# Optimization experiments

Measured on AMD Instinct MI355X. Metric: run time of the kernel, lower is better.

The kernel has to match this reference:

```python
import jax, jax.numpy as jnp
import numpy as np

B, T, N_EMBD, HEAD = 8, 2048, 1024, 64
NEG_INF = -1e30  # stand-in for float('-inf'), safe under fp16/bf16 after where


def setup_inputs() -> dict:
    key = jax.random.key(0)
    k0, k1, k2, k3 = jax.random.split(key, 4)
    idx = jax.random.normal(k0, (B, T, N_EMBD), dtype=jnp.float32)
    # nn.Linear weights have shape (out_features, in_features)
    Wk = jax.random.normal(k1, (HEAD, N_EMBD), dtype=jnp.float32) * 0.02
    Wq = jax.random.normal(k2, (HEAD, N_EMBD), dtype=jnp.float32) * 0.02
    Wv = jax.random.normal(k3, (HEAD, N_EMBD), dtype=jnp.float32) * 0.02
    return {"idx": idx, "Wk": Wk, "Wq": Wq, "Wv": Wv}


def reference(idx, Wk, Wq, Wv):
    # idx: [B,T,C]; W*: [H,C] (torch Linear layout, y = x @ W.T)
    Tn = idx.shape[1]
    k = jnp.einsum('btc,hc->bth', idx, Wk)
    q = jnp.einsum('btc,hc->bth', idx, Wq)
    v = jnp.einsum('btc,hc->bth', idx, Wv)
    # NOTE: original has NO 1/sqrt(head_size) scaling
    wei = jnp.einsum('bth,bsh->bts', q, k)  # [B,T,T]
    causal = jnp.tril(jnp.ones((Tn, Tn), dtype=bool))  # keep where tril != 0
    wei = jnp.where(causal[None, :, :], wei, NEG_INF)
    # NOTE: original softmaxes over dim=1 (query axis), not the last axis
    wei = jax.nn.softmax(wei, axis=1)
    out = jnp.einsum('bts,bsh->bth', wei, v)  # [B,T,H]
    return out
```

## Files before the change

kernel.cpp:

```cpp
#include <hip/hip_runtime.h>


typedef __attribute__((ext_vector_type(8))) short bf16x8;
typedef __attribute__((ext_vector_type(4))) float f32x4;
typedef unsigned short u16;

#define MFMA(a, b, c) __builtin_amdgcn_mfma_f32_16x16x32_bf16((a), (b), (c), 0, 0, 0)

__device__ __forceinline__ u16 f2bf(float x) {
    unsigned u = __float_as_uint(x);
    u += 0x7fff + ((u >> 16) & 1);
    return (u16)(u >> 16);
}
__device__ __forceinline__ float bf2f(u16 h) {
    return __uint_as_float(((unsigned)h) << 16);
}

__device__ __forceinline__ void split8(const f32x4 x0, const f32x4 x1,
                                       bf16x8* hv, bf16x8* lv)
{
    const float f[8] = {x0[0], x0[1], x0[2], x0[3], x1[0], x1[1], x1[2], x1[3]};
    union { unsigned u[4]; bf16x8 v; } H, L;
    #pragma unroll
    for (int j = 0; j < 4; ++j) {
        const unsigned u0 = __float_as_uint(f[2 * j]);
        const unsigned u1 = __float_as_uint(f[2 * j + 1]);
        H.u[j] = __builtin_amdgcn_perm(u1, u0, 0x07060302);
        const float l0 = f[2 * j]     - __uint_as_float(u0 & 0xffff0000u);
        const float l1 = f[2 * j + 1] - __uint_as_float(u1 & 0xffff0000u);
        L.u[j] = __builtin_amdgcn_perm(__float_as_uint(l1), __float_as_uint(l0),
                                       0x07060302);
    }
    *hv = H.v;
    *lv = L.v;
}

typedef const __attribute__((address_space(1))) void* gas_p;
typedef __attribute__((address_space(3))) void* las_p;

#define WH_OFF  0u
#define WL_OFF  (WH_OFF + 192u*1024u*2u)
#define FQH_OFF (WL_OFF + 192u*1024u*2u)
#define FQL_OFF (FQH_OFF + 2u*1024u*1024u)
#define FKH_OFF (FQL_OFF + 2u*1024u*1024u)
#define FKL_OFF (FKH_OFF + 2u*1024u*1024u)
#define VF_OFF  (FKL_OFF + 2u*1024u*1024u)
#define DD_OFF  (VF_OFF + 2u*1024u*1024u)
#define PF_OFF  (DD_OFF + 8u*2048u*4u)

__global__ __launch_bounds__(128) void wsplit_kernel(
    const float* __restrict__ Wk, const float* __restrict__ Wq,
    const float* __restrict__ Wv, u16* __restrict__ FWH, u16* __restrict__ FWL)
{
    const int n = blockIdx.x;
    const int nblk = n >> 4, lr = n & 15;
    const float* src = (n < 64) ? (Wq + (long)n * 1024)
                     : (n < 128) ? (Wk + (long)(n - 64) * 1024)
                                 : (Wv + (long)(n - 128) * 1024);
    const int f = threadIdx.x;
    const int kc = f >> 2, q = f & 3;
    const float4 f0 = *(const float4*)&src[kc * 32 + q * 8];
    const float4 f1 = *(const float4*)&src[kc * 32 + q * 8 + 4];
    const float vs[8] = {f0.x, f0.y, f0.z, f0.w, f1.x, f1.y, f1.z, f1.w};
    bf16x8 hv, lv;
    #pragma unroll
    for (int j = 0; j < 8; ++j) {
        const u16 h = f2bf(vs[j]);
        hv[j] = (short)h;
        lv[j] = (short)f2bf(vs[j] - bf2f(h));
    }
    const long o = ((long)(nblk * 32 + kc) * 64 + q * 16 + lr) * 8;
    *(bf16x8*)&FWH[o] = hv;
    *(bf16x8*)&FWL[o] = lv;
}

__global__ __launch_bounds__(512, 2) void qkv_kernel(
    const float* __restrict__ idx, const u16* __restrict__ FWH, const u16* __restrict__ FWL,
    u16* __restrict__ FQH, u16* __restrict__ FQL,
    u16* __restrict__ FKH, u16* __restrict__ FKL, u16* __restrict__ VF)
{
    __shared__ float a_f0[64 * 128];
    __shared__ float a_f1[64 * 128];
    const int tid = threadIdx.x;
    const int w = tid >> 6, lr = tid & 15, quad = (tid >> 4) & 3;
    const int lane = tid & 63;
    const int r0 = blockIdx.x * 64;
    const int b = r0 >> 11, t0 = r0 & 2047;
    const int m0 = (w & 1) * 32;
    const int nbb = (w >> 1) * 3;

    const float* gsrc[4];
    int lseg[4];
    #pragma unroll
    for (int g = 0; g < 4; ++g) {
        const int s = g * 8 + w;
        const int row = s * 2 + (lane >> 5);
        const int lc = (lane & 31) ^ (row & 7);
        gsrc[g] = idx + (long)(r0 + row) * 1024 + lc * 4;
        lseg[g] = s * 256;
    }

#define STAGE(BUF, IT)                                                        \
    {                                                                         \
        _Pragma("unroll")                                                     \
        for (int g = 0; g < 4; ++g) {                                         \
            __builtin_amdgcn_global_load_lds(                                 \
                (gas_p)(gsrc[g] + (IT) * 128),                                \
                (las_p)(BUF + lseg[g]), 16, 0, 0);                            \
        }                                                                     \
    }

    f32x4 acc[2][3] = {};

    STAGE(a_f0, 0);
    __syncthreads();

#define QKV_ITER(IT, BUF, NXT)                                                \
    {                                                                         \
        const int it_ = (IT);                                                 \
        if (it_ < 7) STAGE(NXT, it_ + 1);                                     \
        _Pragma("unroll")                                                     \
        for (int kblk = 0; kblk < 4; ++kblk) {                                \
            const int kc = it_ * 4 + kblk;                                    \
            bf16x8 AH[2], AL[2];                                              \
            _Pragma("unroll")                                                 \
            for (int mi = 0; mi < 2; ++mi) {                                  \
                const int row = m0 + mi * 16 + lr;                            \
                const int pc0 = (kblk * 8 + quad * 2) ^ (lr & 7);             \
                const f32x4 x0 = *(const f32x4*)&BUF[row * 128 + pc0 * 4];    \
                const f32x4 x1 = *(const f32x4*)&BUF[row * 128 + (pc0 ^ 1) * 4]; \
                split8(x0, x1, &AH[mi], &AL[mi]);                             \
            }                                                                 \
            _Pragma("unroll")                                                 \
            for (int nf = 0; nf < 3; ++nf) {                                  \
                const long fb = (long)(nbb + nf) * 16384 + (long)kc * 512     \
                              + lane * 8;                                     \
                const bf16x8 bh = *(const bf16x8*)&FWH[fb];                   \
                const bf16x8 bl = *(const bf16x8*)&FWL[fb];                   \
                _Pragma("unroll")                                             \
                for (int mi = 0; mi < 2; ++mi) {                              \
                    f32x4 c = acc[mi][nf];                                    \
                    c = MFMA(AH[mi], bh, c);                                  \
                    c = MFMA(AL[mi], bh, c);                                  \
                    c = MFMA(AH[mi], bl, c);                                  \
                    acc[mi][nf] = c;                                          \
                }                                                             \
            }                                                                 \
        }                                                                     \
        if (it_ < 7) __syncthreads();                                         \
    }

    for (int it2 = 0; it2 < 4; ++it2) {
        QKV_ITER(2 * it2,     a_f0, a_f1);
        QKV_ITER(2 * it2 + 1, a_f1, a_f0);
    }
#undef QKV_ITER
#undef STAGE

    #pragma unroll
    for (int mi = 0; mi < 2; ++mi) {
        const int tb = t0 + m0 + mi * 16 + quad * 4;
        const int tblk = (t0 + m0 + mi * 16) >> 4;
        #pragma unroll
        for (int nf = 0; nf < 3; ++nf) {
            const int n = (nbb + nf) * 16 + lr;
            const f32x4 a = acc[mi][nf];
            if (n < 128) {
                u16* Hd = (n < 64) ? FQH : FKH;
                u16* Ld = (n < 64) ? FQL : FKL;
                const int h = n & 63;
                const int kc = h >> 5;
                const int lsub = 16 * ((h & 31) >> 3);
                const long base = ((long)(b * 128 + tblk) * 2 + kc) * 512 + (h & 7);
                #pragma unroll
                for (int r = 0; r < 4; ++r) {
                    const float v = a[r];
                    const u16 hi = f2bf(v);
                    const u16 lo = f2bf(v - bf2f(hi));
                    const long o = base + (long)(quad * 4 + r + lsub) * 8;
                    Hd[o] = hi; Ld[o] = lo;
                }
            } else {
                const int h = n - 128;
                const int hblk = h >> 4;
                #pragma unroll
                for (int r = 0; r < 4; ++r) {
                    const int t = tb + r;
                    const long o = ((long)(b * 4 + hblk) * 64 + (t >> 5)) * 512
                                 + (long)(16 * ((t & 31) >> 3) + (h & 15)) * 8 + (t & 7);
                    VF[o] = f2bf(a[r]);
                }
            }
        }
    }
}

__global__ __launch_bounds__(256, 4) void stats_kernel(
    const u16* __restrict__ FQH, const u16* __restrict__ FQL,
    const u16* __restrict__ FKH, const u16* __restrict__ FKL,
    u16* __restrict__ PF, float* __restrict__ D)
{
    __shared__ float red[4][64];
    const int tid = threadIdx.x;
    const int w = tid >> 6, lr = tid & 15, quad = (tid >> 4) & 3;
    const int lane = tid & 63;
    const int b = blockIdx.y;
    int x = blockIdx.x, i = 0;
    for (;;) { const int nc = (35 - i) >> 2; if (x < nc) break; x -= nc; ++i; }
    const int s0 = i * 64;
    const int jt0 = i + 4 * x, jt1 = min(jt0 + 4, 32);

    bf16x8 BH[4][2], BL[4][2];
    #pragma unroll
    for (int nf = 0; nf < 4; ++nf) {
        const long kb = ((long)(b * 128 + i * 4 + nf) * 2) * 512 + lane * 8;
        BH[nf][0] = *(const bf16x8*)&FKH[kb];
        BH[nf][1] = *(const bf16x8*)&FKH[kb + 512];
        BL[nf][0] = *(const bf16x8*)&FKL[kb];
        BL[nf][1] = *(const bf16x8*)&FKL[kb + 512];
    }

    float dsum[4] = {0.f, 0.f, 0.f, 0.f};
    for (int jt = jt0; jt < jt1; ++jt) {
        const long qb = ((long)(b * 128 + jt * 4 + w) * 2) * 512 + lane * 8;
        const bf16x8 ah0 = *(const bf16x8*)&FQH[qb];
        const bf16x8 ah1 = *(const bf16x8*)&FQH[qb + 512];
        const bf16x8 al0 = *(const bf16x8*)&FQL[qb];
        const bf16x8 al1 = *(const bf16x8*)&FQL[qb + 512];
        const bool diag = (jt == i);
        #pragma unroll
        for (int nf = 0; nf < 4; ++nf) {
            f32x4 cc = {};
            cc = MFMA(ah0, BH[nf][0], cc);
            cc = MFMA(al0, BH[nf][0], cc);
            cc = MFMA(ah0, BL[nf][0], cc);
            cc = MFMA(ah1, BH[nf][1], cc);
            cc = MFMA(al1, BH[nf][1], cc);
            cc = MFMA(ah1, BL[nf][1], cc);

            const long pbase = ((long)(b * 128 + jt * 4 + w) * 64 + i * 2 + (nf >> 1)) * 512
                             + (long)(((nf & 1) * 2 + (lr >> 3)) * 16) * 8 + (lr & 7);
            const int sl = nf * 16 + lr;
            #pragma unroll
            for (int r = 0; r < 4; ++r) {
                float ev = __expf(cc[r]);
                if (diag && (w * 16 + quad * 4 + r < sl)) ev = 0.f;
                dsum[nf] += ev;
                PF[pbase + (long)(quad * 4 + r) * 8] = f2bf(ev);
            }
        }
    }

    #pragma unroll
    for (int nf = 0; nf < 4; ++nf) {
        dsum[nf] += __shfl_xor(dsum[nf], 16);
        dsum[nf] += __shfl_xor(dsum[nf], 32);
    }
    if (quad == 0) {
        #pragma unroll
        for (int nf = 0; nf < 4; ++nf) red[w][nf * 16 + lr] = dsum[nf];
    }
    __syncthreads();
    if (tid < 64)
        atomicAdd(&D[b * 2048 + s0 + tid],
                  red[0][tid] + red[1][tid] + red[2][tid] + red[3][tid]);
}

__global__ __launch_bounds__(256) void vscale_kernel(
    u16* __restrict__ VF, const float* __restrict__ D)
{
    const int g = blockIdx.x * 256 + threadIdx.x;
    const long e = (long)g * 8;
    const int lane = (int)((e >> 3) & 63);
    const int kc   = (int)((e >> 9) & 63);
    const int b    = (int)(e >> 17);
    const int s = kc * 32 + (lane >> 4) * 8;
    const float4 d0 = *(const float4*)&D[b * 2048 + s];
    const float4 d1 = *(const float4*)&D[b * 2048 + s + 4];
    const float dv[8] = {d0.x, d0.y, d0.z, d0.w, d1.x, d1.y, d1.z, d1.w};
    bf16x8 vv = *(bf16x8*)&VF[e];
    bf16x8 ov;
    #pragma unroll
    for (int j = 0; j < 8; ++j)
        ov[j] = (short)f2bf(bf2f((u16)vv[j]) / dv[j]);
    *(bf16x8*)&VF[e] = ov;
}

__global__ __launch_bounds__(256, 4) void out_kernel(
    const u16* __restrict__ PF, const u16* __restrict__ VF,
    float* __restrict__ out)
{
    const int tid = threadIdx.x;
    const int w = tid >> 6, lr = tid & 15, quad = (tid >> 4) & 3;
    const int lane = tid & 63;
    const int b = blockIdx.y;
    int x = blockIdx.x, i = 0;
    for (;;) { const int nc = (i + 8) >> 3; if (x < nc) break; x -= nc; ++i; }
    const int t0 = i * 64;
    const int js0 = 8 * x, js1 = min(8 * x + 8, i + 1);
    const int tblk = i * 4 + w;

    f32x4 oacc[4] = {};
    for (int js = js0; js < js1; ++js) {
        const long pb = ((long)(b * 128 + tblk) * 64 + 2 * js) * 512 + lane * 8;
        const bf16x8 a0 = *(const bf16x8*)&PF[pb];
        const bf16x8 a1 = *(const bf16x8*)&PF[pb + 512];
        #pragma unroll
        for (int nf = 0; nf < 4; ++nf) {
            const long vb = ((long)(b * 4 + nf) * 64 + 2 * js) * 512 + lane * 8;
            const bf16x8 v0 = *(const bf16x8*)&VF[vb];
            const bf16x8 v1 = *(const bf16x8*)&VF[vb + 512];
            oacc[nf] = MFMA(a0, v0, oacc[nf]);
            oacc[nf] = MFMA(a1, v1, oacc[nf]);
        }
    }

    const bool single = (i < 8);
    #pragma unroll
    for (int nf = 0; nf < 4; ++nf) {
        const int h = nf * 16 + lr;
        #pragma unroll
        for (int r = 0; r < 4; ++r) {
            const int t = t0 + w * 16 + quad * 4 + r;
            const long o = (long)(b * 2048 + t) * 64 + h;
            if (single) out[o] = oacc[nf][r];
            else        atomicAdd(&out[o], oacc[nf][r]);
        }
    }
}

extern "C" void kernel_launch(void* const* d_in, const int* in_sizes, int n_in,
                              void* d_out, int out_size, void* d_ws, size_t ws_size,
                              hipStream_t stream)
{
    const float* idx = (const float*)d_in[0];
    const float* Wk  = (const float*)d_in[1];
    const float* Wq  = (const float*)d_in[2];
    const float* Wv  = (const float*)d_in[3];
    char* ws = (char*)d_ws;
    float* out = (float*)d_out;

    u16* FWH = (u16*)(ws + WH_OFF);  u16* FWL = (u16*)(ws + WL_OFF);
    u16* FQH = (u16*)(ws + FQH_OFF); u16* FQL = (u16*)(ws + FQL_OFF);
    u16* FKH = (u16*)(ws + FKH_OFF); u16* FKL = (u16*)(ws + FKL_OFF);
    u16* VF  = (u16*)(ws + VF_OFF);
    float* Dp = (float*)(ws + DD_OFF);
    u16* PF  = (u16*)(ws + PF_OFF);

    hipMemsetAsync(out, 0, (size_t)8 * 2048 * 64 * sizeof(float), stream);
    hipMemsetAsync(Dp, 0, (size_t)8 * 2048 * sizeof(float), stream);

    wsplit_kernel<<<192, 128, 0, stream>>>(Wk, Wq, Wv, FWH, FWL);
    qkv_kernel<<<256, 512, 0, stream>>>(idx, FWH, FWL, FQH, FQL, FKH, FKL, VF);
    stats_kernel<<<dim3(144, 8), 256, 0, stream>>>(FQH, FQL, FKH, FKL, PF, Dp);
    vscale_kernel<<<512, 256, 0, stream>>>(VF, Dp);
    out_kernel<<<dim3(80, 8), 256, 0, stream>>>(PF, VF, out);
}
```

Measured before the change: 171.6 us.

## Stage QKV weight fragments through LDS with four-deep async pipeline

The QKV projection kernel now streams both the input rows and the pre-split bf16 hi/lo weight fragments into shared memory with global_load_lds, using a 4-buffer ring over 32 k-chunks of 32 columns. Previously only the activations went through a double buffer and the weights were loaded directly from global memory, which exposed global latency inside the MFMA loop. Explicit vmcnt waits and barriers replace the per-iteration syncthreads, keeping three stages of loads in flight. Shared memory use grows to 128 KB per block, which may limit occupancy under the two-blocks-per-CU launch bound, and there are more, finer-grained barriers.

Result: faster. 161.8 us (-5.7%).

```diff
diff --git a/kernel.cpp b/kernel.cpp
--- a/kernel.cpp
+++ b/kernel.cpp
@@ -79,8 +79,7 @@
     u16* __restrict__ FQH, u16* __restrict__ FQL,
     u16* __restrict__ FKH, u16* __restrict__ FKL, u16* __restrict__ VF)
 {
-    __shared__ float a_f0[64 * 128];
-    __shared__ float a_f1[64 * 128];
+    __shared__ __align__(16) char smem[4][32768];
     const int tid = threadIdx.x;
     const int w = tid >> 6, lr = tid & 15, quad = (tid >> 4) & 3;
     const int lane = tid & 63;
@@ -89,73 +88,91 @@
     const int m0 = (w & 1) * 32;
     const int nbb = (w >> 1) * 3;
 
-    const float* gsrc[4];
-    int lseg[4];
-    #pragma unroll
-    for (int g = 0; g < 4; ++g) {
-        const int s = g * 8 + w;
-        const int row = s * 2 + (lane >> 5);
-        const int lc = (lane & 31) ^ (row & 7);
-        gsrc[g] = idx + (long)(r0 + row) * 1024 + lc * 4;
-        lseg[g] = s * 256;
-    }
-
-#define STAGE(BUF, IT)                                                        \
+    const int arow = w * 8 + (lane >> 3);
+    const int achk = (lane & 7) ^ (lane >> 3);
+    const float* asrc = idx + (long)(r0 + arow) * 1024 + achk * 4;
+
+    const u16* fsrc[3];
+    int fdst[3];
+    #pragma unroll
+    for (int j = 0; j < 3; ++j) {
+        const int seg = w * 3 + j;
+        const int nblk = seg >> 1, hl = seg & 1;
+        fsrc[j] = (hl ? FWL : FWH) + (long)nblk * 16384 + lane * 8;
+        fdst[j] = seg * 512;
+    }
+
+#define ABUF(NB) ((float*)(smem[NB]))
+#define FBUF(NB) ((u16*)(smem[(NB)] + 8192))
+
+#define ISSUE(PH)                                                             \
     {                                                                         \
+        const int nb_ = (PH) & 3;                                             \
+        __builtin_amdgcn_global_load_lds((gas_p)(asrc + (PH) * 32),           \
+            (las_p)(ABUF(nb_) + w * 256), 16, 0, 0);                          \
         _Pragma("unroll")                                                     \
-        for (int g = 0; g < 4; ++g) {                                         \
-            __builtin_amdgcn_global_load_lds(                                 \
-                (gas_p)(gsrc[g] + (IT) * 128),                                \
-                (las_p)(BUF + lseg[g]), 16, 0, 0);                            \
+        for (int j = 0; j < 3; ++j)                                           \
+            __builtin_amdgcn_global_load_lds((gas_p)(fsrc[j] + (long)(PH) * 512), \
+                (las_p)(FBUF(nb_) + fdst[j]), 16, 0, 0);                      \
+    }
+
+#define COMPUTE(PH)                                                           \
+    {                                                                         \
+        const int nb_ = (PH) & 3;                                             \
+        const float* A_ = ABUF(nb_);                                          \
+        const u16* F_ = FBUF(nb_);                                            \
+        bf16x8 AH[2], AL[2];                                                  \
+        _Pragma("unroll")                                                     \
+        for (int mi = 0; mi < 2; ++mi) {                                      \
+            const int R = m0 + mi * 16 + lr;                                  \
+            const int c0 = (quad * 2) ^ (lr & 7);                             \
+            const f32x4 x0 = *(const f32x4*)&A_[R * 32 + c0 * 4];             \
+            const f32x4 x1 = *(const f32x4*)&A_[R * 32 + (c0 ^ 1) * 4];       \
+            split8(x0, x1, &AH[mi], &AL[mi]);                                 \
         }                                                                     \
-    }
-
-    f32x4 acc[2][3] = {};
-
-    STAGE(a_f0, 0);
-    __syncthreads();
-
-#define QKV_ITER(IT, BUF, NXT)                                                \
-    {                                                                         \
-        const int it_ = (IT);                                                 \
-        if (it_ < 7) STAGE(NXT, it_ + 1);                                     \
         _Pragma("unroll")                                                     \
-        for (int kblk = 0; kblk < 4; ++kblk) {                                \
-            const int kc = it_ * 4 + kblk;                                    \
-            bf16x8 AH[2], AL[2];                                              \
+        for (int nf = 0; nf < 3; ++nf) {                                      \
+            const int sb = ((nbb + nf) * 2) * 512 + lane * 8;                 \
+            const bf16x8 bh = *(const bf16x8*)&F_[sb];                        \
+            const bf16x8 bl = *(const bf16x8*)&F_[sb + 512];                  \
             _Pragma("unroll")                                                 \
             for (int mi = 0; mi < 2; ++mi) {                                  \
-                const int row = m0 + mi * 16 + lr;                            \
-                const int pc0 = (kblk * 8 + quad * 2) ^ (lr & 7);             \
-                const f32x4 x0 = *(const f32x4*)&BUF[row * 128 + pc0 * 4];    \
-                const f32x4 x1 = *(const f32x4*)&BUF[row * 128 + (pc0 ^ 1) * 4]; \
-                split8(x0, x1, &AH[mi], &AL[mi]);                             \
-            }                                                                 \
-            _Pragma("unroll")                                                 \
-            for (int nf = 0; nf < 3; ++nf) {                                  \
-                const long fb = (long)(nbb + nf) * 16384 + (long)kc * 512     \
-                              + lane * 8;                                     \
-                const bf16x8 bh = *(const bf16x8*)&FWH[fb];                   \
-                const bf16x8 bl = *(const bf16x8*)&FWL[fb];                   \
-                _Pragma("unroll")                                             \
-                for (int mi = 0; mi < 2; ++mi) {                              \
-                    f32x4 c = acc[mi][nf];                                    \
-                    c = MFMA(AH[mi], bh, c);                                  \
-                    c = MFMA(AL[mi], bh, c);                                  \
-                    c = MFMA(AH[mi], bl, c);                                  \
-                    acc[mi][nf] = c;                                          \
-                }                                                             \
+                f32x4 c = acc[mi][nf];                                        \
+                c = MFMA(AH[mi], bh, c);                                      \
+                c = MFMA(AL[mi], bh, c);                                      \
+                c = MFMA(AH[mi], bl, c);                                      \
+                acc[mi][nf] = c;                                              \
             }                                                                 \
         }                                                                     \
-        if (it_ < 7) __syncthreads();                                         \
-    }
-
-    for (int it2 = 0; it2 < 4; ++it2) {
-        QKV_ITER(2 * it2,     a_f0, a_f1);
-        QKV_ITER(2 * it2 + 1, a_f1, a_f0);
-    }
-#undef QKV_ITER
-#undef STAGE
+    }
+
+#define WAITV(N)                                                              \
+    asm volatile("s_waitcnt vmcnt(" #N ")" ::: "memory");                     \
+    __builtin_amdgcn_sched_barrier(0);                                        \
+    __builtin_amdgcn_s_barrier();
+
+    f32x4 acc[2][3] = {};
+
+    ISSUE(0); ISSUE(1); ISSUE(2);
+    WAITV(8)
+
+    for (int ph = 0; ph < 29; ++ph) {
+        ISSUE(ph + 3);
+        __builtin_amdgcn_sched_barrier(0);
+        COMPUTE(ph);
+        WAITV(8)
+    }
+    COMPUTE(29);
+    WAITV(4)
+    COMPUTE(30);
+    WAITV(0)
+    COMPUTE(31);
+
+#undef WAITV
+#undef COMPUTE
+#undef ISSUE
+#undef ABUF
+#undef FBUF
 
     #pragma unroll
     for (int mi = 0; mi < 2; ++mi) {
```

## Drop weight low-part split and triple-buffer QKV loads through LDS

Applied to the files above, without the earlier changes.

Weights are now stored only as a single bf16 high part, so the QKV projection runs two MFMAs per tile (A-high and A-low times W-high) instead of three. The activation tiles and the weight fragments are both staged into LDS with async global-to-LDS loads in a 3-deep ring, using explicit vmcnt waits and barriers in place of the old double buffer with weights read straight from global. The aim is to cut MFMA count and global weight traffic and to hide load latency better. In exchange the weights lose precision, and LDS use grows to 120KB per block, which may limit occupancy.

After: 153.8 us. 10.4% less time.

```diff
diff --git a/kernel.cpp b/kernel.cpp
--- a/kernel.cpp
+++ b/kernel.cpp
@@ -50,7 +50,7 @@
 
 __global__ __launch_bounds__(128) void wsplit_kernel(
     const float* __restrict__ Wk, const float* __restrict__ Wq,
-    const float* __restrict__ Wv, u16* __restrict__ FWH, u16* __restrict__ FWL)
+    const float* __restrict__ Wv, u16* __restrict__ FWH)
 {
     const int n = blockIdx.x;
     const int nblk = n >> 4, lr = n & 15;
@@ -62,25 +62,19 @@
     const float4 f0 = *(const float4*)&src[kc * 32 + q * 8];
     const float4 f1 = *(const float4*)&src[kc * 32 + q * 8 + 4];
     const float vs[8] = {f0.x, f0.y, f0.z, f0.w, f1.x, f1.y, f1.z, f1.w};
-    bf16x8 hv, lv;
-    #pragma unroll
-    for (int j = 0; j < 8; ++j) {
-        const u16 h = f2bf(vs[j]);
-        hv[j] = (short)h;
-        lv[j] = (short)f2bf(vs[j] - bf2f(h));
-    }
+    bf16x8 hv;
+    #pragma unroll
+    for (int j = 0; j < 8; ++j) hv[j] = (short)f2bf(vs[j]);
     const long o = ((long)(nblk * 32 + kc) * 64 + q * 16 + lr) * 8;
     *(bf16x8*)&FWH[o] = hv;
-    *(bf16x8*)&FWL[o] = lv;
 }
 
 __global__ __launch_bounds__(512, 2) void qkv_kernel(
-    const float* __restrict__ idx, const u16* __restrict__ FWH, const u16* __restrict__ FWL,
+    const float* __restrict__ idx, const u16* __restrict__ FWH,
     u16* __restrict__ FQH, u16* __restrict__ FQL,
     u16* __restrict__ FKH, u16* __restrict__ FKL, u16* __restrict__ VF)
 {
-    __shared__ float a_f0[64 * 128];
-    __shared__ float a_f1[64 * 128];
+    __shared__ __align__(16) char smem[3][40960];
     const int tid = threadIdx.x;
     const int w = tid >> 6, lr = tid & 15, quad = (tid >> 4) & 3;
     const int lane = tid & 63;
@@ -89,73 +83,93 @@
     const int m0 = (w & 1) * 32;
     const int nbb = (w >> 1) * 3;
 
-    const float* gsrc[4];
-    int lseg[4];
-    #pragma unroll
-    for (int g = 0; g < 4; ++g) {
-        const int s = g * 8 + w;
-        const int row = s * 2 + (lane >> 5);
-        const int lc = (lane & 31) ^ (row & 7);
-        gsrc[g] = idx + (long)(r0 + row) * 1024 + lc * 4;
-        lseg[g] = s * 256;
-    }
-
-#define STAGE(BUF, IT)                                                        \
+    const float* asrc[2];
+    int adst[2];
+    #pragma unroll
+    for (int j = 0; j < 2; ++j) {
+        const int s = w * 2 + j;
+        const int row = s * 4 + (lane >> 4);
+        const int lc = (lane & 15) ^ (row & 7);
+        asrc[j] = idx + (long)(r0 + row) * 1024 + lc * 4;
+        adst[j] = s * 1024;
+    }
+    const u16* fsrc[3];
+    int fdst[3];
+    #pragma unroll
+    for (int j = 0; j < 3; ++j) {
+        const int seg = w * 3 + j;
+        const int nblk = seg >> 1, kcl = seg & 1;
+        fsrc[j] = FWH + (long)nblk * 16384 + kcl * 512 + lane * 8;
+        fdst[j] = 16384 + seg * 1024;
+    }
+
+#define ISSUE(PH)                                                             \
     {                                                                         \
+        const int nb_ = (PH) % 3;                                             \
         _Pragma("unroll")                                                     \
-        for (int g = 0; g < 4; ++g) {                                         \
-            __builtin_amdgcn_global_load_lds(                                 \
-                (gas_p)(gsrc[g] + (IT) * 128),                                \
-                (las_p)(BUF + lseg[g]), 16, 0, 0);                            \
-        }                                                                     \
-    }
-
-    f32x4 acc[2][3] = {};
-
-    STAGE(a_f0, 0);
-    __syncthreads();
-
-#define QKV_ITER(IT, BUF, NXT)                                                \
+        for (int j = 0; j < 2; ++j)                                           \
+            __builtin_amdgcn_global_load_lds((gas_p)(asrc[j] + (PH) * 64),    \
+                (las_p)(smem[nb_] + adst[j]), 16, 0, 0);                      \
+        _Pragma("unroll")                                                     \
+        for (int j = 0; j < 3; ++j)                                           \
+            __builtin_amdgcn_global_load_lds((gas_p)(fsrc[j] + (long)(PH) * 1024), \
+                (las_p)(smem[nb_] + fdst[j]), 16, 0, 0);                      \
+    }
+
+#define COMPUTE(PH)                                                           \
     {                                                                         \
-        const int it_ = (IT);                                                 \
-        if (it_ < 7) STAGE(NXT, it_ + 1);                                     \
+        const int nb_ = (PH) % 3;                                             \
+        const float* A_ = (const float*)smem[nb_];                            \
+        const u16* F_ = (const u16*)(smem[nb_] + 16384);                      \
         _Pragma("unroll")                                                     \
-        for (int kblk = 0; kblk < 4; ++kblk) {                                \
-            const int kc = it_ * 4 + kblk;                                    \
+        for (int kc = 0; kc < 2; ++kc) {                                      \
             bf16x8 AH[2], AL[2];                                              \
             _Pragma("unroll")                                                 \
             for (int mi = 0; mi < 2; ++mi) {                                  \
-                const int row = m0 + mi * 16 + lr;                            \
-                const int pc0 = (kblk * 8 + quad * 2) ^ (lr & 7);             \
-                const f32x4 x0 = *(const f32x4*)&BUF[row * 128 + pc0 * 4];    \
-                const f32x4 x1 = *(const f32x4*)&BUF[row * 128 + (pc0 ^ 1) * 4]; \
+                const int R = m0 + mi * 16 + lr;                              \
+                const int c0 = (kc * 8 + quad * 2) ^ (lr & 7);                \
+                const f32x4 x0 = *(const f32x4*)&A_[R * 64 + c0 * 4];         \
+                const f32x4 x1 = *(const f32x4*)&A_[R * 64 + (c0 ^ 1) * 4];   \
                 split8(x0, x1, &AH[mi], &AL[mi]);                             \
             }                                                                 \
             _Pragma("unroll")                                                 \
             for (int nf = 0; nf < 3; ++nf) {                                  \
-                const long fb = (long)(nbb + nf) * 16384 + (long)kc * 512     \
-                              + lane * 8;                                     \
-                const bf16x8 bh = *(const bf16x8*)&FWH[fb];                   \
-                const bf16x8 bl = *(const bf16x8*)&FWL[fb];                   \
+                const int sb = (((nbb + nf) * 2 + kc)) * 512 + lane * 8;      \
+                const bf16x8 bh = *(const bf16x8*)&F_[sb];                    \
                 _Pragma("unroll")                                             \
                 for (int mi = 0; mi < 2; ++mi) {                              \
                     f32x4 c = acc[mi][nf];                                    \
                     c = MFMA(AH[mi], bh, c);                                  \
                     c = MFMA(AL[mi], bh, c);                                  \
-                    c = MFMA(AH[mi], bl, c);                                  \
                     acc[mi][nf] = c;                                          \
                 }                                                             \
             }                                                                 \
         }                                                                     \
-        if (it_ < 7) __syncthreads();                                         \
-    }
-
-    for (int it2 = 0; it2 < 4; ++it2) {
-        QKV_ITER(2 * it2,     a_f0, a_f1);
-        QKV_ITER(2 * it2 + 1, a_f1, a_f0);
-    }
-#undef QKV_ITER
-#undef STAGE
+    }
+
+#define WAITV(N)                                                              \
+    asm volatile("s_waitcnt vmcnt(" #N ")" ::: "memory");                     \
+    __builtin_amdgcn_sched_barrier(0);                                        \
+    __builtin_amdgcn_s_barrier();
+
+    f32x4 acc[2][3] = {};
+
+    ISSUE(0); ISSUE(1);
+    WAITV(5)
+
+    for (int ph = 0; ph < 14; ++ph) {
+        ISSUE(ph + 2);
+        __builtin_amdgcn_sched_barrier(0);
+        COMPUTE(ph);
+        WAITV(5)
+    }
+    COMPUTE(14);
+    WAITV(0)
+    COMPUTE(15);
+
+#undef WAITV
+#undef COMPUTE
+#undef ISSUE
 
     #pragma unroll
     for (int mi = 0; mi < 2; ++mi) {
@@ -340,7 +354,7 @@
     char* ws = (char*)d_ws;
     float* out = (float*)d_out;
 
-    u16* FWH = (u16*)(ws + WH_OFF);  u16* FWL = (u16*)(ws + WL_OFF);
+    u16* FWH = (u16*)(ws + WH_OFF);
     u16* FQH = (u16*)(ws + FQH_OFF); u16* FQL = (u16*)(ws + FQL_OFF);
     u16* FKH = (u16*)(ws + FKH_OFF); u16* FKL = (u16*)(ws + FKL_OFF);
     u16* VF  = (u16*)(ws + VF_OFF);
@@ -350,8 +364,8 @@
     hipMemsetAsync(out, 0, (size_t)8 * 2048 * 64 * sizeof(float), stream);
     hipMemsetAsync(Dp, 0, (size_t)8 * 2048 * sizeof(float), stream);
 
-    wsplit_kernel<<<192, 128, 0, stream>>>(Wk, Wq, Wv, FWH, FWL);
-    qkv_kernel<<<256, 512, 0, stream>>>(idx, FWH, FWL, FQH, FQL, FKH, FKL, VF);
+    wsplit_kernel<<<192, 128, 0, stream>>>(Wk, Wq, Wv, FWH);
+    qkv_kernel<<<256, 512, 0, stream>>>(idx, FWH, FQH, FQL, FKH, FKL, VF);
     stats_kernel<<<dim3(144, 8), 256, 0, stream>>>(FQH, FQL, FKH, FKL, PF, Dp);
     vscale_kernel<<<512, 256, 0, stream>>>(VF, Dp);
     out_kernel<<<dim3(80, 8), 256, 0, stream>>>(PF, VF, out);
```
